# Kernel optimization log

Hardware: AMD Instinct MI355X
Metric: run time of the kernel (lower is better)

Reference implementation:

```python
import jax, jax.numpy as jnp
import numpy as np

L = 16            # number of levels
F = 2             # features per level
T = 1 << 17       # hashmap size per level (power of 2)
N_TREES = 8       # forest blocks
N = 2_000_000     # query points
RES = np.array([16, 22, 30, 41, 55, 75, 102, 139, 188, 256, 348, 472, 642, 872, 1184, 1608], dtype=np.int64)
# 8 trilinear corner offsets [8,3]
OFFS = np.stack(np.meshgrid([0, 1], [0, 1], [0, 1], indexing='ij'), axis=-1).reshape(8, 3).astype(np.int32)
PRIMES = (np.uint32(1), np.uint32(2654435761), np.uint32(805459861))


def _hash(coords):
    # coords: [N,8,3] int32 grid corner coords -> [N,8] table index (NGP spatial hash)
    c = coords.astype(jnp.uint32)
    h = (c[..., 0] * PRIMES[0]) ^ (c[..., 1] * PRIMES[1]) ^ (c[..., 2] * PRIMES[2])
    return (h & jnp.uint32(T - 1)).astype(jnp.int32)


def setup_inputs() -> dict:
    key = jax.random.key(0)
    k1, k2, k3 = jax.random.split(key, 3)
    block_x = jax.random.uniform(k1, (N, 3), minval=-1.0, maxval=1.0, dtype=jnp.float32)
    bound = 1e-4
    params = jax.random.uniform(k2, (N_TREES, L, T, F), minval=-bound, maxval=bound, dtype=jnp.float32)
    block_inds = jax.random.randint(k3, (N,), 0, N_TREES)
    return {"block_x": block_x, "params": params, "block_inds": block_inds}


def reference(block_x, params, block_inds):
    # block_x in [-1,1]^3 -> [0,1]^3 (matches `block_x / 2.0 + 0.5` in forward)
    x01 = block_x * 0.5 + 0.5
    offs = jnp.asarray(OFFS)                    # [8,3]
    offs_b = jnp.asarray(OFFS, dtype=bool)      # [8,3]
    outs = []
    for l in range(L):
        R = int(RES[l])
        pos = x01 * (R - 1)                     # [N,3]
        p0 = jnp.floor(pos)
        w = pos - p0                            # trilinear fracs [N,3]
        p0i = p0.astype(jnp.int32)
        corners = jnp.clip(p0i[:, None, :] + offs[None], 0, R - 1)   # [N,8,3]
        idx = _hash(corners)                                          # [N,8]
        feats = params[block_inds[:, None], l, idx, :]                # [N,8,F] per-tree gather
        wc = jnp.prod(jnp.where(offs_b[None], w[:, None, :], 1.0 - w[:, None, :]), axis=-1)  # [N,8]
        outs.append(jnp.einsum('nc,ncf->nf', wc, feats))              # [N,F]
    return jnp.concatenate(outs, axis=-1)        # [N, L*F]
```

## Files before the change

### kernel.cpp

```cpp
#include <hip/hip_runtime.h>

#define NLEVELS 16
#define TSIZE 131072
#define TMASK (TSIZE - 1)
#define NBUCK 32768

typedef float f32x4 __attribute__((ext_vector_type(4)));

__device__ __constant__ float RM1_TAB[16] = {
    15.f, 21.f, 29.f, 40.f, 54.f, 74.f, 101.f, 138.f,
    187.f, 255.f, 347.f, 471.f, 641.f, 871.f, 1183.f, 1607.f
};

__device__ __forceinline__ unsigned spread4(unsigned v) {
    v = (v | (v << 4)) & 0x0C3u;
    v = (v | (v << 2)) & 0x249u;
    return v;
}

__device__ __forceinline__ unsigned bucket_key(float x, float y, float z, unsigned tree) {
    const int cx = min(max((int)((x * 0.5f + 0.5f) * 16.f), 0), 15);
    const int cy = min(max((int)((y * 0.5f + 0.5f) * 16.f), 0), 15);
    const int cz = min(max((int)((z * 0.5f + 0.5f) * 16.f), 0), 15);
    const unsigned m = spread4((unsigned)cx) | (spread4((unsigned)cy) << 1)
                     | (spread4((unsigned)cz) << 2);
    return (tree << 12) | m;
}


__global__ __launch_bounds__(256) void k_hist(const float* __restrict__ xs,
                                              const int* __restrict__ inds, int N,
                                              unsigned* __restrict__ hist) {
    const int i = blockIdx.x * 256 + threadIdx.x;
    if (i >= N) return;
    const unsigned key = bucket_key(xs[3 * i], xs[3 * i + 1], xs[3 * i + 2],
                                    (unsigned)(inds[i] & 7));
    atomicAdd(&hist[key], 1u);
}

__global__ __launch_bounds__(1024) void k_scan(const unsigned* __restrict__ hist,
                                               unsigned* __restrict__ cursor) {
    __shared__ unsigned sums[1024];
    const int t = threadIdx.x;
    const int per = NBUCK / 1024;
    unsigned s = 0;
    #pragma unroll
    for (int j = 0; j < per; ++j) s += hist[t * per + j];
    sums[t] = s;
    __syncthreads();
    for (int off = 1; off < 1024; off <<= 1) {
        const unsigned add = (t >= off) ? sums[t - off] : 0u;
        __syncthreads();
        sums[t] += add;
        __syncthreads();
    }
    unsigned run = (t == 0) ? 0u : sums[t - 1];
    #pragma unroll
    for (int j = 0; j < per; ++j) {
        cursor[t * per + j] = run;
        run += hist[t * per + j];
    }
}

__global__ __launch_bounds__(256) void k_scatter(const float* __restrict__ xs,
                                                 const int* __restrict__ inds, int N,
                                                 unsigned* __restrict__ cursor,
                                                 float4* __restrict__ sorted) {
    const int i = blockIdx.x * 256 + threadIdx.x;
    if (i >= N) return;
    const float x = xs[3 * i], y = xs[3 * i + 1], z = xs[3 * i + 2];
    const unsigned tree = (unsigned)(inds[i] & 7);
    const unsigned key = bucket_key(x, y, z, tree);
    const unsigned pos = atomicAdd(&cursor[key], 1u);
    sorted[pos] = make_float4(x, y, z, __uint_as_float(((unsigned)i) | (tree << 24)));
}


__global__ __launch_bounds__(256) void k_main(const float4* __restrict__ sorted,
                                              const float* __restrict__ params,
                                              float4* __restrict__ ws2,
                                              float4* __restrict__ out4,
                                              int N, int nc, int direct) {
    const int b = blockIdx.x;
    const int j = b & 7;
    const int chunk = b >> 3;
    const int i = chunk * 256 + threadIdx.x;
    if (i >= N) return;

    const float4 p = sorted[i];
    const unsigned wbits = __float_as_uint(p.w);
    const int n = (int)(wbits & 0xFFFFFFu);
    const int tree = (int)(wbits >> 24);

    const int levels[2] = { j, 15 - j };
    float acc[4];

    #pragma unroll
    for (int kk = 0; kk < 2; ++kk) {
        const int l = levels[kk];
        const float rm1 = RM1_TAB[l];
        const int rmax = (int)rm1;

        const float px = (p.x * 0.5f + 0.5f) * rm1;
        const float py = (p.y * 0.5f + 0.5f) * rm1;
        const float pz = (p.z * 0.5f + 0.5f) * rm1;
        const float fx = floorf(px), fy = floorf(py), fz = floorf(pz);
        const float wx = px - fx, wy = py - fy, wz = pz - fz;
        const int ix = (int)fx, iy = (int)fy, iz = (int)fz;

        const int x0 = min(max(ix, 0), rmax), x1 = min(max(ix + 1, 0), rmax);
        const int y0 = min(max(iy, 0), rmax), y1 = min(max(iy + 1, 0), rmax);
        const int z0 = min(max(iz, 0), rmax), z1 = min(max(iz + 1, 0), rmax);

        const unsigned hx0 = (unsigned)x0;
        const unsigned hx1 = (unsigned)x1;
        const unsigned hy0 = (unsigned)y0 * 2654435761u;
        const unsigned hy1 = (unsigned)y1 * 2654435761u;
        const unsigned hz0 = (unsigned)z0 * 805459861u;
        const unsigned hz1 = (unsigned)z1 * 805459861u;

        const float2* __restrict__ tbl =
            (const float2*)(params + (size_t)(tree * NLEVELS + l) * (TSIZE * 2));

        const unsigned m00 = hy0 ^ hz0;
        const unsigned m01 = hy0 ^ hz1;
        const unsigned m10 = hy1 ^ hz0;
        const unsigned m11 = hy1 ^ hz1;
        const unsigned i000 = (hx0 ^ m00) & TMASK;
        const unsigned i001 = (hx0 ^ m01) & TMASK;
        const unsigned i010 = (hx0 ^ m10) & TMASK;
        const unsigned i011 = (hx0 ^ m11) & TMASK;

        float2 f000, f001, f010, f011, f100, f101, f110, f111;

        const bool pairOK = ((x0 & 1) == 0) && (x1 == x0 + 1);
        if (pairOK) {
            const float4* __restrict__ tbl4 = (const float4*)tbl;
            const float4 q00 = tbl4[i000 >> 1];
            const float4 q01 = tbl4[i001 >> 1];
            const float4 q10 = tbl4[i010 >> 1];
            const float4 q11 = tbl4[i011 >> 1];
            f000 = (i000 & 1) ? make_float2(q00.z, q00.w) : make_float2(q00.x, q00.y);
            f100 = (i000 & 1) ? make_float2(q00.x, q00.y) : make_float2(q00.z, q00.w);
            f001 = (i001 & 1) ? make_float2(q01.z, q01.w) : make_float2(q01.x, q01.y);
            f101 = (i001 & 1) ? make_float2(q01.x, q01.y) : make_float2(q01.z, q01.w);
            f010 = (i010 & 1) ? make_float2(q10.z, q10.w) : make_float2(q10.x, q10.y);
            f110 = (i010 & 1) ? make_float2(q10.x, q10.y) : make_float2(q10.z, q10.w);
            f011 = (i011 & 1) ? make_float2(q11.z, q11.w) : make_float2(q11.x, q11.y);
            f111 = (i011 & 1) ? make_float2(q11.x, q11.y) : make_float2(q11.z, q11.w);
        } else {
            const unsigned i100 = (hx1 ^ m00) & TMASK;
            const unsigned i101 = (hx1 ^ m01) & TMASK;
            const unsigned i110 = (hx1 ^ m10) & TMASK;
            const unsigned i111 = (hx1 ^ m11) & TMASK;
            f000 = tbl[i000]; f001 = tbl[i001];
            f010 = tbl[i010]; f011 = tbl[i011];
            f100 = tbl[i100]; f101 = tbl[i101];
            f110 = tbl[i110]; f111 = tbl[i111];
        }

        const float wx0 = 1.f - wx, wy0 = 1.f - wy, wz0 = 1.f - wz;

        const float w000 = wx0 * wy0 * wz0;
        const float w001 = wx0 * wy0 * wz;
        const float w010 = wx0 * wy  * wz0;
        const float w011 = wx0 * wy  * wz;
        const float w100 = wx  * wy0 * wz0;
        const float w101 = wx  * wy0 * wz;
        const float w110 = wx  * wy  * wz0;
        const float w111 = wx  * wy  * wz;

        float a0 = 0.f, a1 = 0.f;
        a0 = fmaf(w000, f000.x, a0); a1 = fmaf(w000, f000.y, a1);
        a0 = fmaf(w001, f001.x, a0); a1 = fmaf(w001, f001.y, a1);
        a0 = fmaf(w010, f010.x, a0); a1 = fmaf(w010, f010.y, a1);
        a0 = fmaf(w011, f011.x, a0); a1 = fmaf(w011, f011.y, a1);
        a0 = fmaf(w100, f100.x, a0); a1 = fmaf(w100, f100.y, a1);
        a0 = fmaf(w101, f101.x, a0); a1 = fmaf(w101, f101.y, a1);
        a0 = fmaf(w110, f110.x, a0); a1 = fmaf(w110, f110.y, a1);
        a0 = fmaf(w111, f111.x, a0); a1 = fmaf(w111, f111.y, a1);

        acc[2 * kk + 0] = a0;
        acc[2 * kk + 1] = a1;
    }

    if (direct) {
        ((float2*)out4)[(size_t)n * 16 + levels[0]] = make_float2(acc[0], acc[1]);
        ((float2*)out4)[(size_t)n * 16 + levels[1]] = make_float2(acc[2], acc[3]);
    } else {
        const float4 v = make_float4(acc[0], acc[1], acc[2], acc[3]);
        const size_t stride = (size_t)nc * 256;
        __builtin_nontemporal_store(*(const f32x4*)&v,
                                    (f32x4*)&ws2[(size_t)j * stride + i]);
    }
}


__global__ __launch_bounds__(256) void k_final(const float4* __restrict__ sorted,
                                               const float4* __restrict__ ws2,
                                               float4* __restrict__ out4,
                                               int N, int nc) {
    const int i = blockIdx.x * 256 + threadIdx.x;
    if (i >= N) return;
    const unsigned wbits = __float_as_uint(sorted[i].w);
    const int n = (int)(wbits & 0xFFFFFFu);
    const size_t stride = (size_t)nc * 256;

    float4 q[8];
    #pragma unroll
    for (int j = 0; j < 8; ++j) {
        f32x4 v = __builtin_nontemporal_load((const f32x4*)&ws2[(size_t)j * stride + i]);
        q[j] = *(const float4*)&v;
    }
    #pragma unroll
    for (int kk = 0; kk < 8; ++kk) {
        float4 o;
        if (kk < 4) {
            o = make_float4(q[2 * kk].x, q[2 * kk].y, q[2 * kk + 1].x, q[2 * kk + 1].y);
        } else {
            o = make_float4(q[15 - 2 * kk].z, q[15 - 2 * kk].w,
                            q[14 - 2 * kk].z, q[14 - 2 * kk].w);
        }
        out4[(size_t)n * 8 + kk] = o;
    }
}


__global__ __launch_bounds__(256) void lotd_fwd_fused(
    const float* __restrict__ xs, const float* __restrict__ params,
    const int* __restrict__ inds, float* __restrict__ out, int N)
{
    const int g = blockIdx.x * 256 + threadIdx.x;
    const int n = g >> 4;
    if (n >= N) return;
    const int l = g & 15;
    const float rm1 = RM1_TAB[l];
    const int rmax = (int)rm1;
    const float x = xs[3 * n], y = xs[3 * n + 1], z = xs[3 * n + 2];
    const int tree = inds[n];
    const float px = (x * 0.5f + 0.5f) * rm1;
    const float py = (y * 0.5f + 0.5f) * rm1;
    const float pz = (z * 0.5f + 0.5f) * rm1;
    const float fx = floorf(px), fy = floorf(py), fz = floorf(pz);
    const float wx = px - fx, wy = py - fy, wz = pz - fz;
    const int ix = (int)fx, iy = (int)fy, iz = (int)fz;
    const int x0 = min(max(ix, 0), rmax), x1 = min(max(ix + 1, 0), rmax);
    const int y0 = min(max(iy, 0), rmax), y1 = min(max(iy + 1, 0), rmax);
    const int z0 = min(max(iz, 0), rmax), z1 = min(max(iz + 1, 0), rmax);
    const unsigned hx0 = (unsigned)x0, hx1 = (unsigned)x1;
    const unsigned hy0 = (unsigned)y0 * 2654435761u, hy1 = (unsigned)y1 * 2654435761u;
    const unsigned hz0 = (unsigned)z0 * 805459861u,  hz1 = (unsigned)z1 * 805459861u;
    const float2* tbl = (const float2*)(params + (size_t)(tree * NLEVELS + l) * (TSIZE * 2));
    const float2 f000 = tbl[(hx0 ^ hy0 ^ hz0) & TMASK];
    const float2 f001 = tbl[(hx0 ^ hy0 ^ hz1) & TMASK];
    const float2 f010 = tbl[(hx0 ^ hy1 ^ hz0) & TMASK];
    const float2 f011 = tbl[(hx0 ^ hy1 ^ hz1) & TMASK];
    const float2 f100 = tbl[(hx1 ^ hy0 ^ hz0) & TMASK];
    const float2 f101 = tbl[(hx1 ^ hy0 ^ hz1) & TMASK];
    const float2 f110 = tbl[(hx1 ^ hy1 ^ hz0) & TMASK];
    const float2 f111 = tbl[(hx1 ^ hy1 ^ hz1) & TMASK];
    const float wx0 = 1.f - wx, wy0 = 1.f - wy, wz0 = 1.f - wz;
    float a0 = 0.f, a1 = 0.f;
    a0 = fmaf(wx0*wy0*wz0, f000.x, a0); a1 = fmaf(wx0*wy0*wz0, f000.y, a1);
    a0 = fmaf(wx0*wy0*wz , f001.x, a0); a1 = fmaf(wx0*wy0*wz , f001.y, a1);
    a0 = fmaf(wx0*wy *wz0, f010.x, a0); a1 = fmaf(wx0*wy *wz0, f010.y, a1);
    a0 = fmaf(wx0*wy *wz , f011.x, a0); a1 = fmaf(wx0*wy *wz , f011.y, a1);
    a0 = fmaf(wx *wy0*wz0, f100.x, a0); a1 = fmaf(wx *wy0*wz0, f100.y, a1);
    a0 = fmaf(wx *wy0*wz , f101.x, a0); a1 = fmaf(wx *wy0*wz , f101.y, a1);
    a0 = fmaf(wx *wy *wz0, f110.x, a0); a1 = fmaf(wx *wy *wz0, f110.y, a1);
    a0 = fmaf(wx *wy *wz , f111.x, a0); a1 = fmaf(wx *wy *wz , f111.y, a1);
    ((float2*)out)[(size_t)n * 16 + l] = make_float2(a0, a1);
}

extern "C" void kernel_launch(void* const* d_in, const int* in_sizes, int n_in,
                              void* d_out, int out_size, void* d_ws, size_t ws_size,
                              hipStream_t stream) {
    const float* xs     = (const float*)d_in[0];
    const float* params = (const float*)d_in[1];
    const int*   inds   = (const int*)d_in[2];
    float*       out    = (float*)d_out;

    const int N = in_sizes[0] / 3;
    const int nc = (N + 255) / 256;

    const size_t hist_bytes   = (size_t)NBUCK * 4;
    const size_t head_bytes   = 2 * hist_bytes;
    const size_t sorted_bytes = ((size_t)N * 16 + 255) & ~(size_t)255;
    const size_t ws2_bytes    = (size_t)nc * 256 * 8 * 16;
    const size_t need_B = head_bytes + sorted_bytes;
    const size_t need_A = need_B + ws2_bytes;

    if (ws_size < need_B) {
        const int total = N * NLEVELS;
        lotd_fwd_fused<<<(total + 255) / 256, 256, 0, stream>>>(xs, params, inds, out, N);
        return;
    }

    unsigned* hist   = (unsigned*)d_ws;
    unsigned* cursor = (unsigned*)((char*)d_ws + hist_bytes);
    float4*   sorted = (float4*)((char*)d_ws + head_bytes);
    float4*   ws2    = (float4*)((char*)d_ws + head_bytes + sorted_bytes);

    hipMemsetAsync(hist, 0, hist_bytes, stream);
    k_hist<<<nc, 256, 0, stream>>>(xs, inds, N, hist);
    k_scan<<<1, 1024, 0, stream>>>(hist, cursor);
    k_scatter<<<nc, 256, 0, stream>>>(xs, inds, N, cursor, sorted);

    const int direct = (ws_size < need_A) ? 1 : 0;
    k_main<<<nc * 8, 256, 0, stream>>>(sorted, params,
                                       direct ? nullptr : ws2,
                                       (float4*)out, N, nc, direct);
    if (!direct)
        k_final<<<nc, 256, 0, stream>>>(sorted, ws2, (float4*)out, N, nc);
}
```

Baseline: 835.0 us.

## Convert main gather kernel to persistent blocks with atomic work queues per level pair

```diff
diff --git a/kernel.cpp b/kernel.cpp
--- a/kernel.cpp
+++ b/kernel.cpp
@@ -76,15 +76,13 @@
 }
 
 
-__global__ __launch_bounds__(256) void k_main(const float4* __restrict__ sorted,
-                                              const float* __restrict__ params,
-                                              float4* __restrict__ ws2,
-                                              float4* __restrict__ out4,
-                                              int N, int nc, int direct) {
-    const int b = blockIdx.x;
-    const int j = b & 7;
-    const int chunk = b >> 3;
-    const int i = chunk * 256 + threadIdx.x;
+__device__ __forceinline__ void do_task(const float4* __restrict__ sorted,
+                                        const float* __restrict__ params,
+                                        float4* __restrict__ ws2,
+                                        float4* __restrict__ out4,
+                                        int N, int nc, int direct,
+                                        int v, int t) {
+    const int i = t * 256 + (int)threadIdx.x;
     if (i >= N) return;
 
     const float4 p = sorted[i];
@@ -92,7 +90,7 @@
     const int n = (int)(wbits & 0xFFFFFFu);
     const int tree = (int)(wbits >> 24);
 
-    const int levels[2] = { j, 15 - j };
+    const int levels[2] = { v, 15 - v };
     float acc[4];
 
     #pragma unroll
@@ -188,10 +186,33 @@
         ((float2*)out4)[(size_t)n * 16 + levels[0]] = make_float2(acc[0], acc[1]);
         ((float2*)out4)[(size_t)n * 16 + levels[1]] = make_float2(acc[2], acc[3]);
     } else {
-        const float4 v = make_float4(acc[0], acc[1], acc[2], acc[3]);
+        const float4 o = make_float4(acc[0], acc[1], acc[2], acc[3]);
         const size_t stride = (size_t)nc * 256;
-        __builtin_nontemporal_store(*(const f32x4*)&v,
-                                    (f32x4*)&ws2[(size_t)j * stride + i]);
+        __builtin_nontemporal_store(*(const f32x4*)&o,
+                                    (f32x4*)&ws2[(size_t)v * stride + i]);
+    }
+}
+
+
+__global__ __launch_bounds__(256) void k_main(const float4* __restrict__ sorted,
+                                              const float* __restrict__ params,
+                                              float4* __restrict__ ws2,
+                                              float4* __restrict__ out4,
+                                              unsigned* __restrict__ q,
+                                              int N, int nc, int direct) {
+    __shared__ unsigned s_t;
+    const int j = blockIdx.x & 7;
+
+    for (int v0 = 0; v0 < 8; ++v0) {
+        const int v = (j + v0) & 7;
+        for (;;) {
+            if (threadIdx.x == 0) s_t = atomicAdd(&q[v], 1u);
+            __syncthreads();
+            const unsigned t = s_t;
+            __syncthreads();
+            if (t >= (unsigned)nc) break;
+            do_task(sorted, params, ws2, out4, N, nc, direct, v, (int)t);
+        }
     }
 }
 
@@ -284,7 +305,8 @@
     const int nc = (N + 255) / 256;
 
     const size_t hist_bytes   = (size_t)NBUCK * 4;
-    const size_t head_bytes   = 2 * hist_bytes;
+    const size_t q_bytes      = 256;
+    const size_t head_bytes   = hist_bytes + q_bytes + hist_bytes;
     const size_t sorted_bytes = ((size_t)N * 16 + 255) & ~(size_t)255;
     const size_t ws2_bytes    = (size_t)nc * 256 * 8 * 16;
     const size_t need_B = head_bytes + sorted_bytes;
@@ -297,19 +319,20 @@
     }
 
     unsigned* hist   = (unsigned*)d_ws;
-    unsigned* cursor = (unsigned*)((char*)d_ws + hist_bytes);
+    unsigned* q      = (unsigned*)((char*)d_ws + hist_bytes);
+    unsigned* cursor = (unsigned*)((char*)d_ws + hist_bytes + q_bytes);
     float4*   sorted = (float4*)((char*)d_ws + head_bytes);
     float4*   ws2    = (float4*)((char*)d_ws + head_bytes + sorted_bytes);
 
-    hipMemsetAsync(hist, 0, hist_bytes, stream);
+    hipMemsetAsync(hist, 0, hist_bytes + q_bytes, stream);
     k_hist<<<nc, 256, 0, stream>>>(xs, inds, N, hist);
     k_scan<<<1, 1024, 0, stream>>>(hist, cursor);
     k_scatter<<<nc, 256, 0, stream>>>(xs, inds, N, cursor, sorted);
 
     const int direct = (ws_size < need_A) ? 1 : 0;
-    k_main<<<nc * 8, 256, 0, stream>>>(sorted, params,
-                                       direct ? nullptr : ws2,
-                                       (float4*)out, N, nc, direct);
+    k_main<<<2048, 256, 0, stream>>>(sorted, params,
+                                     direct ? nullptr : ws2,
+                                     (float4*)out, q, N, nc, direct);
     if (!direct)
         k_final<<<nc, 256, 0, stream>>>(sorted, ws2, (float4*)out, N, nc);
 }
```

After: 1.292 ms. 1.55x slower.
